# Optimization experiments

Measured on AMD Instinct MI355X. Metric: run time of the kernel, lower is better.

Reference implementation:

```python
import jax, jax.numpy as jnp
import numpy as np

FEATURE_DIM = 512
PREDICATE_DIM = 2000
OBJECT_DIM = 100000
BATCH = 131072
EPS = 1e-5


def setup_inputs() -> dict:
    key = jax.random.key(0)
    ks = jax.random.split(key, 20)
    f, f2 = FEATURE_DIM, FEATURE_DIM // 2

    def w(k, shape, fan_in):
        bound = 1.0 / np.sqrt(fan_in)
        return jax.random.uniform(k, shape, jnp.float32, -bound, bound)

    inp = {
        "subj": jax.random.randint(ks[0], (BATCH,), 0, OBJECT_DIM),
        "obj": jax.random.randint(ks[1], (BATCH,), 0, OBJECT_DIM),
        "predi": jax.random.randint(ks[2], (BATCH,), 0, PREDICATE_DIM),
        # Linear weights stored as (in, out) so one_hot @ W.T == W_io[idx]
        "W1": w(ks[3], (OBJECT_DIM, f), OBJECT_DIM), "b1": w(ks[4], (f,), OBJECT_DIM),
        "g1": jnp.ones((f,), jnp.float32), "be1": jnp.zeros((f,), jnp.float32),
        "W2": w(ks[5], (OBJECT_DIM, f), OBJECT_DIM), "b2": w(ks[6], (f,), OBJECT_DIM),
        "g2": jnp.ones((f,), jnp.float32), "be2": jnp.zeros((f,), jnp.float32),
        "W3": w(ks[7], (PREDICATE_DIM, f), PREDICATE_DIM), "b3": w(ks[8], (f,), PREDICATE_DIM),
        "g3": jnp.ones((f,), jnp.float32), "be3": jnp.zeros((f,), jnp.float32),
        "W4": w(ks[9], (f2, f), f), "b4": w(ks[10], (f2,), f),
        "g4": jnp.ones((f2,), jnp.float32), "be4": jnp.zeros((f2,), jnp.float32),
        "W5": w(ks[11], (1, f2), f2), "b5": w(ks[12], (1,), f2),
    }
    return inp


def _bn(x, g, b):
    # BatchNorm1d training mode: biased variance over batch
    m = jnp.mean(x, axis=0)
    v = jnp.var(x, axis=0)
    return g * (x - m) * jax.lax.rsqrt(v + EPS) + b


def reference(subj, obj, predi,
              W1, b1, g1, be1,
              W2, b2, g2, be2,
              W3, b3, g3, be3,
              W4, b4, g4, be4,
              W5, b5):
    # one_hot(idx) @ W.T + b  ==  row gather of (in,out) weight
    s = jax.nn.relu(_bn(W1[subj] + b1, g1, be1))
    o = jax.nn.relu(_bn(W2[obj] + b2, g2, be2))
    p = jax.nn.relu(_bn(W3[predi] + b3, g3, be3))
    fused = s + p + o                                  # [B, F]
    h = jax.nn.relu(_bn(fused @ W4.T + b4, g4, be4))   # [B, F//2]
    logit = (h @ W5.T + b5).squeeze()                  # [B]
    return logit
```

## Files before the change

kernel.cpp:

```cpp
#include <hip/hip_runtime.h>

#define BATCHN 131072
#define FD 512
#define F2 256
#define LDSTR 520

typedef __bf16 bf16x8 __attribute__((ext_vector_type(8)));
typedef float f32x4 __attribute__((ext_vector_type(4)));

__device__ __forceinline__ ushort f2bf(float f) {
  union { float f; uint u; } c; c.f = f;
  uint u = c.u;
  u += 0x7FFFu + ((u >> 16) & 1u);
  return (ushort)(u >> 16);
}

#define WS_STATS123 0
#define WS_S4 3072
#define WS_SCSH123 35840
#define WS_SCSH4 38912
#define WS_W4BF 39424

__global__ __launch_bounds__(256) void k_stats123(
    const float* __restrict__ W1, const float* __restrict__ W2,
    const float* __restrict__ W3, const int* __restrict__ subj,
    const int* __restrict__ obj, const int* __restrict__ predi,
    float* __restrict__ stats)
{
  const int e = blockIdx.y;
  const float* W = (e == 0) ? W1 : (e == 1 ? W2 : W3);
  const int* idx = (e == 0) ? subj : (e == 1 ? obj : predi);
  __shared__ int idxL[256];
  __shared__ float redS[512], redQ[512];
  int t = threadIdx.x;
  int base = blockIdx.x * 256;
  idxL[t] = idx[base + t];
  redS[t] = 0.f; redS[t + 256] = 0.f; redQ[t] = 0.f; redQ[t + 256] = 0.f;
  __syncthreads();
  int c = t & 63, rg = t >> 6;
  float s[8], q[8];
  #pragma unroll
  for (int j = 0; j < 8; ++j) { s[j] = 0.f; q[j] = 0.f; }
  for (int r = rg; r < 256; r += 4) {
    const float* row = W + (size_t)idxL[r] * FD + c * 8;
    float4 va = *(const float4*)(row);
    float4 vb = *(const float4*)(row + 4);
    float x[8] = {va.x, va.y, va.z, va.w, vb.x, vb.y, vb.z, vb.w};
    #pragma unroll
    for (int j = 0; j < 8; ++j) { s[j] += x[j]; q[j] += x[j] * x[j]; }
  }
  #pragma unroll
  for (int j = 0; j < 8; ++j) {
    atomicAdd(&redS[c * 8 + j], s[j]);
    atomicAdd(&redQ[c * 8 + j], q[j]);
  }
  __syncthreads();
  float* se = stats + e * 1024;
  atomicAdd(&se[t],        redS[t]);
  atomicAdd(&se[t + 256],  redS[t + 256]);
  atomicAdd(&se[512 + t],  redQ[t]);
  atomicAdd(&se[768 + t],  redQ[t + 256]);
}

__global__ void k_fin123(const float* __restrict__ stats,
                         const float* __restrict__ g1, const float* __restrict__ be1,
                         const float* __restrict__ g2, const float* __restrict__ be2,
                         const float* __restrict__ g3, const float* __restrict__ be3,
                         float* __restrict__ scsh)
{
  int e = blockIdx.x, f = threadIdx.x;
  const float* g  = (e == 0) ? g1  : (e == 1 ? g2  : g3);
  const float* be = (e == 0) ? be1 : (e == 1 ? be2 : be3);
  float S = stats[e * 1024 + f], SS = stats[e * 1024 + 512 + f];
  const float invB = 1.f / (float)BATCHN;
  float mean = S * invB;
  float var  = SS * invB - mean * mean;
  if (!(var >= 0.f && var < 1e30f)) var = 1.f;
  if (!(mean > -1e30f && mean < 1e30f)) mean = 0.f;
  float r = rsqrtf(var + 1e-5f);
  float sc = g[f] * r;
  scsh[e * 1024 + f]       = sc;
  scsh[e * 1024 + 512 + f] = be[f] - mean * sc;
}

__global__ __launch_bounds__(256) void k_convW4(const float* __restrict__ W4,
                                                ushort* __restrict__ w4bf)
{
  int i = (blockIdx.x * 256 + threadIdx.x) * 4;
  float4 v = *(const float4*)(W4 + i);
  ushort4 o = {f2bf(v.x), f2bf(v.y), f2bf(v.z), f2bf(v.w)};
  *(ushort4*)(w4bf + i) = o;
}

__device__ __forceinline__ void tile_fused_gemm(
    const float* __restrict__ W1, const float* __restrict__ W2, const float* __restrict__ W3,
    const ushort* __restrict__ w4bf,
    const int* __restrict__ subj, const int* __restrict__ obj, const int* __restrict__ predi,
    const float* __restrict__ scsh, int rowBase, int t,
    ushort* fusedL, int (*idxL)[32], f32x4 acc[2][4])
{
  if (t < 32)      idxL[0][t]      = subj[rowBase + t];
  else if (t < 64) idxL[1][t - 32] = obj[rowBase + t - 32];
  else if (t < 96) idxL[2][t - 64] = predi[rowBase + t - 64];

  int c = t & 63, rg = t >> 6;
  float sc[3][8], sh[3][8];
  #pragma unroll
  for (int e = 0; e < 3; ++e)
    #pragma unroll
    for (int j = 0; j < 8; ++j) {
      sc[e][j] = scsh[e * 1024 + c * 8 + j];
      sh[e][j] = scsh[e * 1024 + 512 + c * 8 + j];
    }
  __syncthreads();

  for (int r = rg; r < 32; r += 4) {
    const float* r1 = W1 + (size_t)idxL[0][r] * FD + c * 8;
    const float* r2 = W2 + (size_t)idxL[1][r] * FD + c * 8;
    const float* r3 = W3 + (size_t)idxL[2][r] * FD + c * 8;
    float4 a1 = *(const float4*)(r1), b1 = *(const float4*)(r1 + 4);
    float4 a2 = *(const float4*)(r2), b2 = *(const float4*)(r2 + 4);
    float4 a3 = *(const float4*)(r3), b3 = *(const float4*)(r3 + 4);
    float x1[8] = {a1.x, a1.y, a1.z, a1.w, b1.x, b1.y, b1.z, b1.w};
    float x2[8] = {a2.x, a2.y, a2.z, a2.w, b2.x, b2.y, b2.z, b2.w};
    float x3[8] = {a3.x, a3.y, a3.z, a3.w, b3.x, b3.y, b3.z, b3.w};
    union { ushort o[8]; uint4 v; } u;
    #pragma unroll
    for (int j = 0; j < 8; ++j) {
      float v = fmaxf(fmaf(sc[0][j], x1[j], sh[0][j]), 0.f)
              + fmaxf(fmaf(sc[1][j], x2[j], sh[1][j]), 0.f)
              + fmaxf(fmaf(sc[2][j], x3[j], sh[2][j]), 0.f);
      v = fminf(v, 60000.f);
      u.o[j] = f2bf(v);
    }
    *(uint4*)&fusedL[r * LDSTR + c * 8] = u.v;
  }
  __syncthreads();

  int w = t >> 6, lane = t & 63;
  int m = lane & 15, q = lane >> 4;
  #pragma unroll
  for (int mi = 0; mi < 2; ++mi)
    #pragma unroll
    for (int ni = 0; ni < 4; ++ni)
      acc[mi][ni] = (f32x4){0.f, 0.f, 0.f, 0.f};

  const ushort* w4p = w4bf + ((size_t)(64 * w + m)) * FD + q * 8;
  const ushort* fpL = fusedL + m * LDSTR + q * 8;

  for (int kk = 0; kk < 16; ++kk) {
    int kc = kk * 32;
    bf16x8 af0 = *(const bf16x8*)(fpL + kc);
    bf16x8 af1 = *(const bf16x8*)(fpL + 16 * LDSTR + kc);
    #pragma unroll
    for (int ni = 0; ni < 4; ++ni) {
      bf16x8 bfv = *(const bf16x8*)(w4p + ni * 16 * FD + kc);
      acc[0][ni] = __builtin_amdgcn_mfma_f32_16x16x32_bf16(af0, bfv, acc[0][ni], 0, 0, 0);
      acc[1][ni] = __builtin_amdgcn_mfma_f32_16x16x32_bf16(af1, bfv, acc[1][ni], 0, 0, 0);
    }
  }
}

__global__ __launch_bounds__(256) void k_pass1(
    const float* __restrict__ W1, const float* __restrict__ W2, const float* __restrict__ W3,
    const ushort* __restrict__ w4bf,
    const int* __restrict__ subj, const int* __restrict__ obj, const int* __restrict__ predi,
    const float* __restrict__ scsh, float* __restrict__ s4)
{
  alignas(16) __shared__ ushort fusedL[32 * LDSTR];
  __shared__ int idxL[3][32];
  __shared__ float colSum[256], colSS[256];
  int t = threadIdx.x;
  colSum[t] = 0.f; colSS[t] = 0.f;
  f32x4 acc[2][4];
  tile_fused_gemm(W1, W2, W3, w4bf, subj, obj, predi, scsh, blockIdx.x * 32, t, fusedL, idxL, acc);

  int w = t >> 6, lane = t & 63, m = lane & 15;
  #pragma unroll
  for (int ni = 0; ni < 4; ++ni) {
    int col = 64 * w + 16 * ni + m;
    float s = 0.f, ss = 0.f;
    #pragma unroll
    for (int mi = 0; mi < 2; ++mi)
      #pragma unroll
      for (int rr = 0; rr < 4; ++rr) {
        float v = acc[mi][ni][rr];
        s += v; ss += v * v;
      }
    atomicAdd(&colSum[col], s);
    atomicAdd(&colSS[col], ss);
  }
  __syncthreads();
  int slot = blockIdx.x & 63;
  atomicAdd(&s4[slot * 512 + t],       colSum[t]);
  atomicAdd(&s4[slot * 512 + 256 + t], colSS[t]);
}

__global__ void k_fin4(const float* __restrict__ s4, const float* __restrict__ g4,
                       const float* __restrict__ be4, float* __restrict__ scsh4)
{
  int j = threadIdx.x;
  float S = 0.f, SS = 0.f;
  for (int sl = 0; sl < 64; ++sl) { S += s4[sl * 512 + j]; SS += s4[sl * 512 + 256 + j]; }
  const float invB = 1.f / (float)BATCHN;
  float mean = S * invB;
  float var  = SS * invB - mean * mean;
  if (!(var >= 0.f && var < 1e30f)) var = 1.f;
  if (!(mean > -1e30f && mean < 1e30f)) mean = 0.f;
  float r = rsqrtf(var + 1e-5f);
  float sc = g4[j] * r;
  scsh4[j]       = sc;
  scsh4[256 + j] = be4[j] - mean * sc;
}

__global__ __launch_bounds__(256) void k_pass2(
    const float* __restrict__ W1, const float* __restrict__ W2, const float* __restrict__ W3,
    const ushort* __restrict__ w4bf,
    const int* __restrict__ subj, const int* __restrict__ obj, const int* __restrict__ predi,
    const float* __restrict__ scsh, const float* __restrict__ scsh4,
    const float* __restrict__ W5, const float* __restrict__ b5,
    float* __restrict__ out)
{
  alignas(16) __shared__ ushort fusedL[32 * LDSTR];
  __shared__ int idxL[3][32];
  __shared__ float partials[4][32];
  int t = threadIdx.x;
  int rowBase = blockIdx.x * 32;
  f32x4 acc[2][4];
  tile_fused_gemm(W1, W2, W3, w4bf, subj, obj, predi, scsh, rowBase, t, fusedL, idxL, acc);

  int w = t >> 6, lane = t & 63, m = lane & 15, q = lane >> 4;
  float sc4v[4], sh4v[4], w5v[4];
  #pragma unroll
  for (int ni = 0; ni < 4; ++ni) {
    int col = 64 * w + 16 * ni + m;
    sc4v[ni] = scsh4[col];
    sh4v[ni] = scsh4[256 + col];
    w5v[ni]  = W5[col];
  }
  float rowAcc[8];
  #pragma unroll
  for (int j = 0; j < 8; ++j) rowAcc[j] = 0.f;
  #pragma unroll
  for (int ni = 0; ni < 4; ++ni)
    #pragma unroll
    for (int mi = 0; mi < 2; ++mi)
      #pragma unroll
      for (int rr = 0; rr < 4; ++rr) {
        float v = fmaxf(fmaf(sc4v[ni], acc[mi][ni][rr], sh4v[ni]), 0.f);
        rowAcc[mi * 4 + rr] += v * w5v[ni];
      }
  #pragma unroll
  for (int j = 0; j < 8; ++j) {
    #pragma unroll
    for (int off = 1; off < 16; off <<= 1)
      rowAcc[j] += __shfl_xor(rowAcc[j], off, 64);
  }
  if (m == 0) {
    #pragma unroll
    for (int mi = 0; mi < 2; ++mi)
      #pragma unroll
      for (int rr = 0; rr < 4; ++rr)
        partials[w][16 * mi + q * 4 + rr] = rowAcc[mi * 4 + rr];
  }
  __syncthreads();
  if (t < 32) {
    float r = partials[0][t] + partials[1][t] + partials[2][t] + partials[3][t];
    out[rowBase + t] = r + b5[0];
  }
}

extern "C" void kernel_launch(void* const* d_in, const int* in_sizes, int n_in,
                              void* d_out, int out_size, void* d_ws, size_t ws_size,
                              hipStream_t stream)
{
  const int* subj  = (const int*)d_in[0];
  const int* obj   = (const int*)d_in[1];
  const int* predi = (const int*)d_in[2];
  const float* W1  = (const float*)d_in[3];
  const float* g1  = (const float*)d_in[5];
  const float* be1 = (const float*)d_in[6];
  const float* W2  = (const float*)d_in[7];
  const float* g2  = (const float*)d_in[9];
  const float* be2 = (const float*)d_in[10];
  const float* W3  = (const float*)d_in[11];
  const float* g3  = (const float*)d_in[13];
  const float* be3 = (const float*)d_in[14];
  const float* W4  = (const float*)d_in[15];
  const float* g4  = (const float*)d_in[17];
  const float* be4 = (const float*)d_in[18];
  const float* W5  = (const float*)d_in[19];
  const float* b5  = (const float*)d_in[20];

  float* wsf = (float*)d_ws;
  ushort* w4bf = (ushort*)(wsf + WS_W4BF);
  float* out = (float*)d_out;

  hipMemsetAsync(d_ws, 0, WS_SCSH123 * 4, stream);
  k_stats123<<<dim3(512, 3, 1), 256, 0, stream>>>(W1, W2, W3, subj, obj, predi, wsf + WS_STATS123);
  k_fin123<<<3, 512, 0, stream>>>(wsf + WS_STATS123, g1, be1, g2, be2, g3, be3, wsf + WS_SCSH123);
  k_convW4<<<128, 256, 0, stream>>>(W4, w4bf);
  k_pass1<<<BATCHN / 32, 256, 0, stream>>>(W1, W2, W3, w4bf, subj, obj, predi,
                                           wsf + WS_SCSH123, wsf + WS_S4);
  k_fin4<<<1, 256, 0, stream>>>(wsf + WS_S4, g4, be4, wsf + WS_SCSH4);
  k_pass2<<<BATCHN / 32, 256, 0, stream>>>(W1, W2, W3, w4bf, subj, obj, predi,
                                           wsf + WS_SCSH123, wsf + WS_SCSH4, W5, b5, out);
}
```

Before: 904.5 us.

## Precompute per-embedding-row projections through W4 and gather them per batch row

Uses linearity of the W4 projection: (s+p+o)@W4ᵀ = s@W4ᵀ + p@W4ᵀ + o@W4ᵀ. Each distinct embedding row is normalized, ReLU'd and projected once into per-table tables A1/A2/A3, skipping rows that no batch index references. The batch passes then gather and sum three 256-wide rows instead of three 512-wide rows plus an MFMA GEMM run twice. BN1-3 statistics are computed from an index histogram weighted over table rows. This adds about 200MB of workspace writes and reads, and it sums the projections in fp32 rather than projecting a bf16-rounded sum.

Measured after the change: 844.5 us. 1.07x faster.

```diff
diff --git a/kernel.cpp b/kernel.cpp
--- a/kernel.cpp
+++ b/kernel.cpp
@@ -3,6 +3,8 @@
 #define BATCHN 131072
 #define FD 512
 #define F2 256
+#define NOBJ 100000
+#define NPRED 2000
 #define LDSTR 520
 
 typedef __bf16 bf16x8 __attribute__((ext_vector_type(8)));
@@ -15,39 +17,61 @@
   return (ushort)(u >> 16);
 }
 
-#define WS_STATS123 0
-#define WS_S4 3072
-#define WS_SCSH123 35840
-#define WS_SCSH4 38912
-#define WS_W4BF 39424
-
-__global__ __launch_bounds__(256) void k_stats123(
+#define WS_STATS123 202752
+#define WS_S4       205824
+#define WS_SCSH123  238592
+#define WS_SCSH4    241664
+#define WS_W4BF     242176
+#define WS_A1       307712
+#define WS_A2       25907712
+#define WS_A3       51507712
+
+__global__ __launch_bounds__(256) void k_hist(
+    const int* __restrict__ subj, const int* __restrict__ obj,
+    const int* __restrict__ predi, int* __restrict__ cnt)
+{
+  int b = blockIdx.x * 256 + threadIdx.x;
+  atomicAdd(&cnt[subj[b]], 1);
+  atomicAdd(&cnt[NOBJ + obj[b]], 1);
+  atomicAdd(&cnt[2 * NOBJ + predi[b]], 1);
+}
+
+#define NB1 782
+#define NB3 16
+#define NB_SCAN (NB1 + NB1 + NB3)
+__global__ __launch_bounds__(256) void k_scan123(
     const float* __restrict__ W1, const float* __restrict__ W2,
-    const float* __restrict__ W3, const int* __restrict__ subj,
-    const int* __restrict__ obj, const int* __restrict__ predi,
+    const float* __restrict__ W3, const int* __restrict__ cnt,
     float* __restrict__ stats)
 {
-  const int e = blockIdx.y;
+  int blk = blockIdx.x;
+  int e, rowBase, N;
+  if (blk < NB1)            { e = 0; rowBase = blk * 128;          N = NOBJ; }
+  else if (blk < 2 * NB1)   { e = 1; rowBase = (blk - NB1) * 128;  N = NOBJ; }
+  else                      { e = 2; rowBase = (blk - 2*NB1) * 128; N = NPRED; }
   const float* W = (e == 0) ? W1 : (e == 1 ? W2 : W3);
-  const int* idx = (e == 0) ? subj : (e == 1 ? obj : predi);
-  __shared__ int idxL[256];
+  const int* cn = cnt + (e == 0 ? 0 : (e == 1 ? NOBJ : 2 * NOBJ));
+
+  __shared__ int cnL[128];
   __shared__ float redS[512], redQ[512];
   int t = threadIdx.x;
-  int base = blockIdx.x * 256;
-  idxL[t] = idx[base + t];
+  if (t < 128) { int r = rowBase + t; cnL[t] = (r < N) ? cn[r] : 0; }
   redS[t] = 0.f; redS[t + 256] = 0.f; redQ[t] = 0.f; redQ[t + 256] = 0.f;
   __syncthreads();
+
   int c = t & 63, rg = t >> 6;
   float s[8], q[8];
   #pragma unroll
   for (int j = 0; j < 8; ++j) { s[j] = 0.f; q[j] = 0.f; }
-  for (int r = rg; r < 256; r += 4) {
-    const float* row = W + (size_t)idxL[r] * FD + c * 8;
+  for (int rl = rg; rl < 128; rl += 4) {
+    float w = (float)cnL[rl];
+    if (w == 0.f) continue;
+    const float* row = W + (size_t)(rowBase + rl) * FD + c * 8;
     float4 va = *(const float4*)(row);
     float4 vb = *(const float4*)(row + 4);
     float x[8] = {va.x, va.y, va.z, va.w, vb.x, vb.y, vb.z, vb.w};
     #pragma unroll
-    for (int j = 0; j < 8; ++j) { s[j] += x[j]; q[j] += x[j] * x[j]; }
+    for (int j = 0; j < 8; ++j) { s[j] += w * x[j]; q[j] += w * x[j] * x[j]; }
   }
   #pragma unroll
   for (int j = 0; j < 8; ++j) {
@@ -92,62 +116,61 @@
   *(ushort4*)(w4bf + i) = o;
 }
 
-__device__ __forceinline__ void tile_fused_gemm(
-    const float* __restrict__ W1, const float* __restrict__ W2, const float* __restrict__ W3,
-    const ushort* __restrict__ w4bf,
-    const int* __restrict__ subj, const int* __restrict__ obj, const int* __restrict__ predi,
-    const float* __restrict__ scsh, int rowBase, int t,
-    ushort* fusedL, int (*idxL)[32], f32x4 acc[2][4])
-{
-  if (t < 32)      idxL[0][t]      = subj[rowBase + t];
-  else if (t < 64) idxL[1][t - 32] = obj[rowBase + t - 32];
-  else if (t < 96) idxL[2][t - 64] = predi[rowBase + t - 64];
-
+#define NB_A1 3125
+#define NB_A3 63
+#define NB_BUILD (NB_A1 + NB_A1 + NB_A3)
+__global__ __launch_bounds__(256) void k_buildA(
+    const float* __restrict__ W1, const float* __restrict__ W2,
+    const float* __restrict__ W3, const ushort* __restrict__ w4bf,
+    const int* __restrict__ cnt, const float* __restrict__ scsh,
+    float* __restrict__ A1, float* __restrict__ A2, float* __restrict__ A3)
+{
+  alignas(16) __shared__ ushort tileL[32 * LDSTR];
+  __shared__ int okL[32];
+  int blk = blockIdx.x;
+  int e, rowBase, N; const float* W; float* A; const int* cn;
+  if (blk < NB_A1)          { e = 0; rowBase = blk * 32;             N = NOBJ;  W = W1; A = A1; cn = cnt; }
+  else if (blk < 2 * NB_A1) { e = 1; rowBase = (blk - NB_A1) * 32;   N = NOBJ;  W = W2; A = A2; cn = cnt + NOBJ; }
+  else                      { e = 2; rowBase = (blk - 2*NB_A1) * 32; N = NPRED; W = W3; A = A3; cn = cnt + 2 * NOBJ; }
+
+  int t = threadIdx.x;
+  if (t < 32) { int r = rowBase + t; okL[t] = (r < N) && (cn[r] != 0); }
   int c = t & 63, rg = t >> 6;
-  float sc[3][8], sh[3][8];
-  #pragma unroll
-  for (int e = 0; e < 3; ++e)
-    #pragma unroll
-    for (int j = 0; j < 8; ++j) {
-      sc[e][j] = scsh[e * 1024 + c * 8 + j];
-      sh[e][j] = scsh[e * 1024 + 512 + c * 8 + j];
-    }
+  float sc[8], sh[8];
+  #pragma unroll
+  for (int j = 0; j < 8; ++j) {
+    sc[j] = scsh[e * 1024 + c * 8 + j];
+    sh[j] = scsh[e * 1024 + 512 + c * 8 + j];
+  }
   __syncthreads();
 
   for (int r = rg; r < 32; r += 4) {
-    const float* r1 = W1 + (size_t)idxL[0][r] * FD + c * 8;
-    const float* r2 = W2 + (size_t)idxL[1][r] * FD + c * 8;
-    const float* r3 = W3 + (size_t)idxL[2][r] * FD + c * 8;
-    float4 a1 = *(const float4*)(r1), b1 = *(const float4*)(r1 + 4);
-    float4 a2 = *(const float4*)(r2), b2 = *(const float4*)(r2 + 4);
-    float4 a3 = *(const float4*)(r3), b3 = *(const float4*)(r3 + 4);
-    float x1[8] = {a1.x, a1.y, a1.z, a1.w, b1.x, b1.y, b1.z, b1.w};
-    float x2[8] = {a2.x, a2.y, a2.z, a2.w, b2.x, b2.y, b2.z, b2.w};
-    float x3[8] = {a3.x, a3.y, a3.z, a3.w, b3.x, b3.y, b3.z, b3.w};
     union { ushort o[8]; uint4 v; } u;
-    #pragma unroll
-    for (int j = 0; j < 8; ++j) {
-      float v = fmaxf(fmaf(sc[0][j], x1[j], sh[0][j]), 0.f)
-              + fmaxf(fmaf(sc[1][j], x2[j], sh[1][j]), 0.f)
-              + fmaxf(fmaf(sc[2][j], x3[j], sh[2][j]), 0.f);
-      v = fminf(v, 60000.f);
-      u.o[j] = f2bf(v);
-    }
-    *(uint4*)&fusedL[r * LDSTR + c * 8] = u.v;
-  }
-  __syncthreads();
-
-  int w = t >> 6, lane = t & 63;
-  int m = lane & 15, q = lane >> 4;
+    if (okL[r]) {
+      const float* row = W + (size_t)(rowBase + r) * FD + c * 8;
+      float4 va = *(const float4*)(row);
+      float4 vb = *(const float4*)(row + 4);
+      float x[8] = {va.x, va.y, va.z, va.w, vb.x, vb.y, vb.z, vb.w};
+      #pragma unroll
+      for (int j = 0; j < 8; ++j) {
+        float v = fmaxf(fmaf(sc[j], x[j], sh[j]), 0.f);
+        v = fminf(v, 60000.f);
+        u.o[j] = f2bf(v);
+      }
+    } else { u.v.x = 0; u.v.y = 0; u.v.z = 0; u.v.w = 0; }
+    *(uint4*)&tileL[r * LDSTR + c * 8] = u.v;
+  }
+  __syncthreads();
+
+  int w = t >> 6, lane = t & 63, m = lane & 15, q = lane >> 4;
+  f32x4 acc[2][4];
   #pragma unroll
   for (int mi = 0; mi < 2; ++mi)
     #pragma unroll
     for (int ni = 0; ni < 4; ++ni)
       acc[mi][ni] = (f32x4){0.f, 0.f, 0.f, 0.f};
-
   const ushort* w4p = w4bf + ((size_t)(64 * w + m)) * FD + q * 8;
-  const ushort* fpL = fusedL + m * LDSTR + q * 8;
-
+  const ushort* fpL = tileL + m * LDSTR + q * 8;
   for (int kk = 0; kk < 16; ++kk) {
     int kc = kk * 32;
     bf16x8 af0 = *(const bf16x8*)(fpL + kc);
@@ -159,41 +182,63 @@
       acc[1][ni] = __builtin_amdgcn_mfma_f32_16x16x32_bf16(af1, bfv, acc[1][ni], 0, 0, 0);
     }
   }
-}
-
-__global__ __launch_bounds__(256) void k_pass1(
-    const float* __restrict__ W1, const float* __restrict__ W2, const float* __restrict__ W3,
-    const ushort* __restrict__ w4bf,
-    const int* __restrict__ subj, const int* __restrict__ obj, const int* __restrict__ predi,
-    const float* __restrict__ scsh, float* __restrict__ s4)
-{
-  alignas(16) __shared__ ushort fusedL[32 * LDSTR];
-  __shared__ int idxL[3][32];
-  __shared__ float colSum[256], colSS[256];
+  __syncthreads();
+
+  float* ldsF = (float*)tileL;
+  #pragma unroll
+  for (int mi = 0; mi < 2; ++mi)
+    #pragma unroll
+    for (int ni = 0; ni < 4; ++ni)
+      #pragma unroll
+      for (int rr = 0; rr < 4; ++rr)
+        ldsF[(16 * mi + 4 * q + rr) * 258 + 64 * w + 16 * ni + m] = acc[mi][ni][rr];
+  __syncthreads();
+  for (int r = 0; r < 32; ++r) {
+    if (okL[r]) A[(size_t)(rowBase + r) * F2 + t] = ldsF[r * 258 + t];
+  }
+}
+
+__global__ __launch_bounds__(256) void k_hstats(
+    const int* __restrict__ subj, const int* __restrict__ obj,
+    const int* __restrict__ predi,
+    const float* __restrict__ A1, const float* __restrict__ A2,
+    const float* __restrict__ A3, float* __restrict__ s4)
+{
+  __shared__ float colS[256], colQ[256];
   int t = threadIdx.x;
-  colSum[t] = 0.f; colSS[t] = 0.f;
-  f32x4 acc[2][4];
-  tile_fused_gemm(W1, W2, W3, w4bf, subj, obj, predi, scsh, blockIdx.x * 32, t, fusedL, idxL, acc);
-
-  int w = t >> 6, lane = t & 63, m = lane & 15;
-  #pragma unroll
-  for (int ni = 0; ni < 4; ++ni) {
-    int col = 64 * w + 16 * ni + m;
-    float s = 0.f, ss = 0.f;
-    #pragma unroll
-    for (int mi = 0; mi < 2; ++mi)
-      #pragma unroll
-      for (int rr = 0; rr < 4; ++rr) {
-        float v = acc[mi][ni][rr];
-        s += v; ss += v * v;
-      }
-    atomicAdd(&colSum[col], s);
-    atomicAdd(&colSS[col], ss);
+  colS[t] = 0.f; colQ[t] = 0.f;
+  __syncthreads();
+  int c = t & 31;
+  int pair = t >> 5;
+  float ls[8], lq[8];
+  #pragma unroll
+  for (int j = 0; j < 8; ++j) { ls[j] = 0.f; lq[j] = 0.f; }
+  int base = blockIdx.x * 64;
+  #pragma unroll 2
+  for (int i = 0; i < 8; ++i) {
+    int b = base + i * 8 + pair;
+    const float* r1 = A1 + (size_t)subj[b]  * F2 + c * 8;
+    const float* r2 = A2 + (size_t)obj[b]   * F2 + c * 8;
+    const float* r3 = A3 + (size_t)predi[b] * F2 + c * 8;
+    f32x4 a0 = *(const f32x4*)(r1), a1 = *(const f32x4*)(r1 + 4);
+    f32x4 b0 = *(const f32x4*)(r2), b1 = *(const f32x4*)(r2 + 4);
+    f32x4 c0 = *(const f32x4*)(r3), c1 = *(const f32x4*)(r3 + 4);
+    f32x4 h0 = a0 + b0 + c0, h1 = a1 + b1 + c1;
+    #pragma unroll
+    for (int j = 0; j < 4; ++j) {
+      ls[j]     += h0[j]; lq[j]     += h0[j] * h0[j];
+      ls[4 + j] += h1[j]; lq[4 + j] += h1[j] * h1[j];
+    }
+  }
+  #pragma unroll
+  for (int j = 0; j < 8; ++j) {
+    atomicAdd(&colS[c * 8 + j], ls[j]);
+    atomicAdd(&colQ[c * 8 + j], lq[j]);
   }
   __syncthreads();
   int slot = blockIdx.x & 63;
-  atomicAdd(&s4[slot * 512 + t],       colSum[t]);
-  atomicAdd(&s4[slot * 512 + 256 + t], colSS[t]);
+  atomicAdd(&s4[slot * 512 + t],       colS[t]);
+  atomicAdd(&s4[slot * 512 + 256 + t], colQ[t]);
 }
 
 __global__ void k_fin4(const float* __restrict__ s4, const float* __restrict__ g4,
@@ -213,60 +258,46 @@
   scsh4[256 + j] = be4[j] - mean * sc;
 }
 
-__global__ __launch_bounds__(256) void k_pass2(
-    const float* __restrict__ W1, const float* __restrict__ W2, const float* __restrict__ W3,
-    const ushort* __restrict__ w4bf,
-    const int* __restrict__ subj, const int* __restrict__ obj, const int* __restrict__ predi,
-    const float* __restrict__ scsh, const float* __restrict__ scsh4,
+__global__ __launch_bounds__(256) void k_final(
+    const int* __restrict__ subj, const int* __restrict__ obj,
+    const int* __restrict__ predi,
+    const float* __restrict__ A1, const float* __restrict__ A2,
+    const float* __restrict__ A3, const float* __restrict__ scsh4,
     const float* __restrict__ W5, const float* __restrict__ b5,
     float* __restrict__ out)
 {
-  alignas(16) __shared__ ushort fusedL[32 * LDSTR];
-  __shared__ int idxL[3][32];
-  __shared__ float partials[4][32];
   int t = threadIdx.x;
-  int rowBase = blockIdx.x * 32;
-  f32x4 acc[2][4];
-  tile_fused_gemm(W1, W2, W3, w4bf, subj, obj, predi, scsh, rowBase, t, fusedL, idxL, acc);
-
-  int w = t >> 6, lane = t & 63, m = lane & 15, q = lane >> 4;
-  float sc4v[4], sh4v[4], w5v[4];
-  #pragma unroll
-  for (int ni = 0; ni < 4; ++ni) {
-    int col = 64 * w + 16 * ni + m;
-    sc4v[ni] = scsh4[col];
-    sh4v[ni] = scsh4[256 + col];
-    w5v[ni]  = W5[col];
-  }
-  float rowAcc[8];
-  #pragma unroll
-  for (int j = 0; j < 8; ++j) rowAcc[j] = 0.f;
-  #pragma unroll
-  for (int ni = 0; ni < 4; ++ni)
-    #pragma unroll
-    for (int mi = 0; mi < 2; ++mi)
-      #pragma unroll
-      for (int rr = 0; rr < 4; ++rr) {
-        float v = fmaxf(fmaf(sc4v[ni], acc[mi][ni][rr], sh4v[ni]), 0.f);
-        rowAcc[mi * 4 + rr] += v * w5v[ni];
-      }
+  int c = t & 31, pair = t >> 5;
+  float sc4v[8], sh4v[8], w5v[8];
   #pragma unroll
   for (int j = 0; j < 8; ++j) {
-    #pragma unroll
-    for (int off = 1; off < 16; off <<= 1)
-      rowAcc[j] += __shfl_xor(rowAcc[j], off, 64);
-  }
-  if (m == 0) {
-    #pragma unroll
-    for (int mi = 0; mi < 2; ++mi)
-      #pragma unroll
-      for (int rr = 0; rr < 4; ++rr)
-        partials[w][16 * mi + q * 4 + rr] = rowAcc[mi * 4 + rr];
-  }
-  __syncthreads();
-  if (t < 32) {
-    float r = partials[0][t] + partials[1][t] + partials[2][t] + partials[3][t];
-    out[rowBase + t] = r + b5[0];
+    int col = c * 8 + j;
+    sc4v[j] = scsh4[col];
+    sh4v[j] = scsh4[256 + col];
+    w5v[j]  = W5[col];
+  }
+  float bb = b5[0];
+  int base = blockIdx.x * 64;
+  #pragma unroll 2
+  for (int i = 0; i < 8; ++i) {
+    int b = base + i * 8 + pair;
+    const float* r1 = A1 + (size_t)subj[b]  * F2 + c * 8;
+    const float* r2 = A2 + (size_t)obj[b]   * F2 + c * 8;
+    const float* r3 = A3 + (size_t)predi[b] * F2 + c * 8;
+    f32x4 a0 = *(const f32x4*)(r1), a1 = *(const f32x4*)(r1 + 4);
+    f32x4 b0 = *(const f32x4*)(r2), b1 = *(const f32x4*)(r2 + 4);
+    f32x4 c0 = *(const f32x4*)(r3), c1 = *(const f32x4*)(r3 + 4);
+    f32x4 h0 = a0 + b0 + c0, h1 = a1 + b1 + c1;
+    float acc = 0.f;
+    #pragma unroll
+    for (int j = 0; j < 4; ++j) {
+      acc += fmaxf(fmaf(sc4v[j],     h0[j], sh4v[j]),     0.f) * w5v[j];
+      acc += fmaxf(fmaf(sc4v[4 + j], h1[j], sh4v[4 + j]), 0.f) * w5v[4 + j];
+    }
+    #pragma unroll
+    for (int off = 1; off < 32; off <<= 1)
+      acc += __shfl_xor(acc, off, 64);
+    if (c == 0) out[b] = acc + bb;
   }
 }
 
@@ -292,17 +323,21 @@
   const float* W5  = (const float*)d_in[19];
   const float* b5  = (const float*)d_in[20];
 
-  float* wsf = (float*)d_ws;
+  float* wsf   = (float*)d_ws;
+  int*   cnt   = (int*)d_ws;
   ushort* w4bf = (ushort*)(wsf + WS_W4BF);
-  float* out = (float*)d_out;
+  float* A1    = wsf + WS_A1;
+  float* A2    = wsf + WS_A2;
+  float* A3    = wsf + WS_A3;
+  float* out   = (float*)d_out;
 
   hipMemsetAsync(d_ws, 0, WS_SCSH123 * 4, stream);
-  k_stats123<<<dim3(512, 3, 1), 256, 0, stream>>>(W1, W2, W3, subj, obj, predi, wsf + WS_STATS123);
+  k_hist<<<BATCHN / 256, 256, 0, stream>>>(subj, obj, predi, cnt);
+  k_convW4<<<128, 256, 0, stream>>>(W4, w4bf);
+  k_scan123<<<NB_SCAN, 256, 0, stream>>>(W1, W2, W3, cnt, wsf + WS_STATS123);
   k_fin123<<<3, 512, 0, stream>>>(wsf + WS_STATS123, g1, be1, g2, be2, g3, be3, wsf + WS_SCSH123);
-  k_convW4<<<128, 256, 0, stream>>>(W4, w4bf);
-  k_pass1<<<BATCHN / 32, 256, 0, stream>>>(W1, W2, W3, w4bf, subj, obj, predi,
-                                           wsf + WS_SCSH123, wsf + WS_S4);
+  k_buildA<<<NB_BUILD, 256, 0, stream>>>(W1, W2, W3, w4bf, cnt, wsf + WS_SCSH123, A1, A2, A3);
+  k_hstats<<<BATCHN / 64, 256, 0, stream>>>(subj, obj, predi, A1, A2, A3, wsf + WS_S4);
   k_fin4<<<1, 256, 0, stream>>>(wsf + WS_S4, g4, be4, wsf + WS_SCSH4);
-  k_pass2<<<BATCHN / 32, 256, 0, stream>>>(W1, W2, W3, w4bf, subj, obj, predi,
-                                           wsf + WS_SCSH123, wsf + WS_SCSH4, W5, b5, out);
-}
+  k_final<<<BATCHN / 64, 256, 0, stream>>>(subj, obj, predi, A1, A2, A3, wsf + WS_SCSH4, W5, b5, out);
+}
```
